# Kernel tuning notes

Measured on AMD Instinct MI355X. Metric: run time of the kernel, lower is better.

## Reference

```python
import jax, jax.numpy as jnp
import numpy as np

ASPECT_RATIOS = jnp.array([0.5, 1.0, 2.0], dtype=jnp.float32)
SCALES = jnp.array([1.0, 2.0, 4.0, 8.0, 16.0], dtype=jnp.float32)
BASE_SIZE = 16
STRIDE = 16
NEG_OVERLAP = 0.3
POS_OVERLAP = 0.7
PADDING = 0.0
RPN_BATCH = 256
RPN_FG_FRACTION = 0.5


def _mkanchors(ws, hs, x_ctr, y_ctr):
    return jnp.stack([x_ctr - 0.5 * (ws - 1), y_ctr - 0.5 * (hs - 1),
                      x_ctr + 0.5 * (ws - 1), y_ctr + 0.5 * (hs - 1)], axis=-1)


def _base_anchors():
    w = h = float(BASE_SIZE)
    x_ctr = y_ctr = 0.5 * (BASE_SIZE - 1)
    size = w * h
    size_ratios = size / ASPECT_RATIOS
    ws = jnp.round(jnp.sqrt(size_ratios))
    hs = jnp.round(ws * ASPECT_RATIOS)
    ratio_anchors = _mkanchors(ws, hs, x_ctr, y_ctr)          # (R,4)
    rw = ratio_anchors[:, 2] - ratio_anchors[:, 0] + 1
    rh = ratio_anchors[:, 3] - ratio_anchors[:, 1] + 1
    rx = ratio_anchors[:, 0] + 0.5 * (rw - 1)
    ry = ratio_anchors[:, 1] + 0.5 * (rh - 1)
    ws2 = rw[:, None] * SCALES[None, :]                        # (R,S)
    hs2 = rh[:, None] * SCALES[None, :]
    anchors = _mkanchors(ws2, hs2, rx[:, None], ry[:, None])   # (R,S,4)
    return anchors.reshape(-1, 4)                              # (A=R*S,4)


def _shifted_anchors(r, c):
    base = _base_anchors()                                     # (A,4)
    sx = jnp.arange(c, dtype=jnp.float32) * STRIDE
    sy = jnp.arange(r, dtype=jnp.float32) * STRIDE
    SX, SY = jnp.meshgrid(sx, sy)                              # (r,c)
    shifts = jnp.stack([SX.ravel(), SY.ravel(), SX.ravel(), SY.ravel()], axis=1)
    return (shifts[:, None, :] + base[None, :, :]).reshape(-1, 4)  # (K=r*c*A,4)


def _iou(a, b):
    area_a = (a[:, 2] - a[:, 0] + 1) * (a[:, 3] - a[:, 1] + 1)
    area_b = (b[:, 2] - b[:, 0] + 1) * (b[:, 3] - b[:, 1] + 1)
    iw = jnp.minimum(a[:, None, 2], b[None, :, 2]) - jnp.maximum(a[:, None, 0], b[None, :, 0]) + 1
    ih = jnp.minimum(a[:, None, 3], b[None, :, 3]) - jnp.maximum(a[:, None, 1], b[None, :, 1]) + 1
    inter = jnp.maximum(iw, 0) * jnp.maximum(ih, 0)
    return inter / (area_a[:, None] + area_b[None, :] - inter)


def _bbox_transform(ex, gt):
    ew = ex[:, 2] - ex[:, 0] + 1.0
    eh = ex[:, 3] - ex[:, 1] + 1.0
    ecx = ex[:, 0] + 0.5 * ew
    ecy = ex[:, 1] + 0.5 * eh
    gw = gt[:, 2] - gt[:, 0] + 1.0
    gh = gt[:, 3] - gt[:, 1] + 1.0
    gcx = gt[:, 0] + 0.5 * gw
    gcy = gt[:, 1] + 0.5 * gh
    return jnp.stack([(gcx - ecx) / ew, (gcy - ecy) / eh,
                      jnp.log(gw / ew), jnp.log(gh / eh)], axis=1)


def reference(target_bounding_boxes, metadata, scores):
    meta = metadata[0]
    gt = target_bounding_boxes[0]                               # (G,4)
    r, c = scores.shape[1], scores.shape[2]
    anchors = _shifted_anchors(r, c)                            # (K,4)
    K = anchors.shape[0]
    h, w = meta[0], meta[1]

    # anchors fully inside the image (padding=0); outside anchors masked
    inside = ((anchors[:, 0] >= -PADDING) & (anchors[:, 1] >= -PADDING) &
              (anchors[:, 2] < w + PADDING) & (anchors[:, 3] < h + PADDING))

    clipped = jnp.stack([jnp.clip(anchors[:, 0], 0.0, w - 1),
                         jnp.clip(anchors[:, 1], 0.0, h - 1),
                         jnp.clip(anchors[:, 2], 0.0, w - 1),
                         jnp.clip(anchors[:, 3], 0.0, h - 1)], axis=1)

    overlaps = _iou(clipped, gt)                                # (K,G)
    overlaps = jnp.where(inside[:, None], overlaps, -1.0)       # ignore outside anchors
    argmax_overlaps = jnp.argmax(overlaps, axis=1)              # best gt per anchor
    max_overlaps = jnp.max(overlaps, axis=1)
    gt_argmax = jnp.argmax(overlaps, axis=0)                    # best anchor per gt

    labels = jnp.full((K,), -1.0, dtype=jnp.float32)
    labels = jnp.where(inside & (max_overlaps < NEG_OVERLAP), 0.0, labels)
    labels = labels.at[gt_argmax].set(1.0)                      # dedup handled by .set
    labels = jnp.where(inside & (max_overlaps >= POS_OVERLAP), 1.0, labels)
    labels = jnp.where(inside, labels, -1.0)                    # unmap fill=-1

    # deterministic subsampling (original shuffles randomly): keep first-by-index
    num_fg = int(RPN_FG_FRACTION * RPN_BATCH)
    pos = labels == 1.0
    pos_rank = jnp.cumsum(pos.astype(jnp.int32))
    labels = jnp.where(pos & (pos_rank > num_fg), -1.0, labels)
    num_pos = jnp.minimum(pos.sum(), num_fg)
    num_bg = RPN_BATCH - num_pos
    neg = labels == 0.0
    neg_rank = jnp.cumsum(neg.astype(jnp.int32))
    labels = jnp.where(neg & (neg_rank > num_bg), -1.0, labels)

    matched_gt = gt[argmax_overlaps]                            # (K,4) gather
    bbox_targets = _bbox_transform(clipped, matched_gt)
    bbox_targets = jnp.where(inside[:, None], bbox_targets, 0.0)  # unmap fill=0

    return anchors[None], bbox_targets[None], labels[None]


def setup_inputs() -> dict:
    key = jax.random.key(0)
    k1, k2 = jax.random.split(key)
    H = W = 1600
    G = 100
    r = c = H // STRIDE                                          # 100
    A = 15                                                       # 3 ratios * 5 scales
    xy = jax.random.uniform(k1, (G, 2), minval=0.0, maxval=1400.0)
    wh = jax.random.uniform(k2, (G, 2), minval=16.0, maxval=200.0)
    gt = jnp.concatenate([xy, xy + wh], axis=1)[None]            # (1,G,4)
    metadata = jnp.array([[float(H), float(W), 1.0]], dtype=jnp.float32)
    scores = jnp.zeros((1, r, c, A), dtype=jnp.float32)          # only shape is used
    return {"target_bounding_boxes": gt, "metadata": metadata, "scores": scores}
```

## Files before the change

### kernel.cpp

```cpp
#include <hip/hip_runtime.h>
#include <math.h>


#define NUM_A 15
#define NUM_FG 128
#define RPN_BATCH 256
#define BLOCK 256
#define BLOCK2 1024
#define M2 2
#define APB2 (BLOCK2 * M2)
#define MAXG 256
#define MAXNG 768
#define CHUNK 8

__device__ __forceinline__ void base_anchor(int a, float& bx1, float& by1,
                                            float& bx2, float& by2) {
    const float RW[3] = {23.f, 16.f, 11.f};
    const float RH[3] = {12.f, 16.f, 22.f};
    int i = a / 5;
    int j = a - i * 5;
    float sc = (float)(1 << j);
    float w = RW[i] * sc;
    float h = RH[i] * sc;
    bx1 = 7.5f - 0.5f * (w - 1.f);
    by1 = 7.5f - 0.5f * (h - 1.f);
    bx2 = 7.5f + 0.5f * (w - 1.f);
    by2 = 7.5f + 0.5f * (h - 1.f);
}

__device__ __forceinline__ void anchor_coords(int k, int c, float& x1, float& y1,
                                              float& x2, float& y2) {
    int a = k % NUM_A;
    int p = k / NUM_A;
    int xi = p % c;
    int yi = p / c;
    float bx1, by1, bx2, by2;
    base_anchor(a, bx1, by1, bx2, by2);
    float sx = (float)xi * 16.f;
    float sy = (float)yi * 16.f;
    x1 = sx + bx1;  y1 = sy + by1;
    x2 = sx + bx2;  y2 = sy + by2;
}

__device__ __forceinline__ unsigned long long packvk(float v, int k) {
    unsigned u = __float_as_uint(v);
    u = (u & 0x80000000u) ? ~u : (u | 0x80000000u);
    return ((unsigned long long)u << 32) | (unsigned)(~k);
}

__global__ void __launch_bounds__(BLOCK) k_main(
        const float* __restrict__ gt, const float* __restrict__ meta,
        float* __restrict__ out_anch, float* __restrict__ out_bb,
        float* __restrict__ out_lab, int* __restrict__ posc, int* __restrict__ negc,
        unsigned long long* __restrict__ pbest, int K, int c, int G) {
    __shared__ float4 s_gt[MAXG];
    __shared__ unsigned long long s_best[MAXG];
    __shared__ int swp[4], swn[4];
    int tid = threadIdx.x;
    int b = blockIdx.x;
    const float4* gtv = (const float4*)gt;
    for (int g = tid; g < G; g += BLOCK) {
        s_gt[g] = gtv[g];
        s_best[g] = 0ULL;
    }
    __syncthreads();

    int k = b * BLOCK + tid;
    bool valid = (k < K);
    float h = meta[0], w = meta[1];
    float wm1 = __fsub_rn(w, 1.f), hm1 = __fsub_rn(h, 1.f);

    float x1, y1, x2, y2;
    anchor_coords(k, c, x1, y1, x2, y2);
    if (valid) ((float4*)out_anch)[k] = make_float4(x1, y1, x2, y2);
    bool inside = (x1 >= 0.f) && (y1 >= 0.f) && (x2 < w) && (y2 < h);

    float cx1 = fminf(fmaxf(x1, 0.f), wm1);
    float cy1 = fminf(fmaxf(y1, 0.f), hm1);
    float cx2 = fminf(fmaxf(x2, 0.f), wm1);
    float cy2 = fminf(fmaxf(y2, 0.f), hm1);
    float area_a = __fmul_rn(__fadd_rn(__fsub_rn(cx2, cx1), 1.f),
                             __fadd_rn(__fsub_rn(cy2, cy1), 1.f));

    float maxv = -2.f;
    int arg = 0;
    if (valid && inside) {
        for (int g = 0; g < G; ++g) {
            float4 gb = s_gt[g];
            float iw = __fadd_rn(__fsub_rn(fminf(cx2, gb.z), fmaxf(cx1, gb.x)), 1.f);
            float ih = __fadd_rn(__fsub_rn(fminf(cy2, gb.w), fmaxf(cy1, gb.y)), 1.f);
            float inter = __fmul_rn(fmaxf(iw, 0.f), fmaxf(ih, 0.f));
            float v = 0.f;
            if (inter > 0.f) {
                float gw = __fadd_rn(__fsub_rn(gb.z, gb.x), 1.f);
                float gh = __fadd_rn(__fsub_rn(gb.w, gb.y), 1.f);
                float areab = __fmul_rn(gw, gh);
                float denom = __fsub_rn(__fadd_rn(area_a, areab), inter);
                v = __fdiv_rn(inter, denom);
                unsigned long long pk = packvk(v, k);
                unsigned cur_hi = ((volatile unsigned*)&s_best[g])[1];
                if ((unsigned)(pk >> 32) >= cur_hi)
                    atomicMax(&s_best[g], pk);
            }
            if (v > maxv) { maxv = v; arg = g; }
        }
    }

    float labf = -1.f;
    if (valid) {
        float t0 = 0.f, t1 = 0.f, t2 = 0.f, t3 = 0.f;
        if (inside) {
            labf = (maxv >= 0.7f) ? 1.f : (maxv < 0.3f ? 0.f : -1.f);
            float4 gb = s_gt[arg];
            float ew  = __fadd_rn(__fsub_rn(cx2, cx1), 1.f);
            float eh  = __fadd_rn(__fsub_rn(cy2, cy1), 1.f);
            float ecx = __fadd_rn(cx1, __fmul_rn(0.5f, ew));
            float ecy = __fadd_rn(cy1, __fmul_rn(0.5f, eh));
            float gw  = __fadd_rn(__fsub_rn(gb.z, gb.x), 1.f);
            float gh  = __fadd_rn(__fsub_rn(gb.w, gb.y), 1.f);
            float gcx = __fadd_rn(gb.x, __fmul_rn(0.5f, gw));
            float gcy = __fadd_rn(gb.y, __fmul_rn(0.5f, gh));
            t0 = __fdiv_rn(__fsub_rn(gcx, ecx), ew);
            t1 = __fdiv_rn(__fsub_rn(gcy, ecy), eh);
            t2 = logf(__fdiv_rn(gw, ew));
            t3 = logf(__fdiv_rn(gh, eh));
        }
        ((float4*)out_bb)[k] = make_float4(t0, t1, t2, t3);
        out_lab[k] = labf;
    }

    bool pos = valid && (labf == 1.f);
    bool neg = valid && (labf == 0.f);
    unsigned long long bp = __ballot(pos ? 1 : 0);
    unsigned long long bn = __ballot(neg ? 1 : 0);
    int lane = tid & 63, wid = tid >> 6;
    if (lane == 0) { swp[wid] = __popcll(bp); swn[wid] = __popcll(bn); }
    __syncthreads();
    if (tid == 0) {
        posc[b] = swp[0] + swp[1] + swp[2] + swp[3];
        negc[b] = swn[0] + swn[1] + swn[2] + swn[3];
    }
    for (int g = tid; g < G; g += BLOCK)
        pbest[(size_t)b * G + g] = s_best[g];
}

__global__ void __launch_bounds__(BLOCK2) k_tail(
        float* __restrict__ out_lab, const int* __restrict__ posc,
        const int* __restrict__ negc, const unsigned long long* __restrict__ pbest,
        int K, int G, int NG) {
    __shared__ unsigned long long s_best[MAXG];
    __shared__ int s_kstar[MAXG];
    __shared__ int s_off_p[MAXNG], s_off_n[MAXNG];
    __shared__ int sp[BLOCK2], sn[BLOCK2];
    __shared__ unsigned char s_star[APB2];
    __shared__ int s_nbg;
    __shared__ int swp[16], swn[16];
    int tid = threadIdx.x;
    int b = blockIdx.x;
    int base = b * APB2;

    for (int i = tid; i < MAXNG; i += BLOCK2) { s_off_p[i] = 0; s_off_n[i] = 0; }
    for (int i = tid; i < APB2; i += BLOCK2) s_star[i] = 0;
    for (int g = tid; g < G; g += BLOCK2) s_best[g] = 0ULL;
    __syncthreads();

    int NT = NG * G;
    int R = BLOCK2 % G;
    int jr[CHUNK];
    jr[0] = 0;
    #pragma unroll
    for (int j = 1; j < CHUNK; ++j) {
        jr[j] = jr[j - 1] + R;
        if (jr[j] >= G) jr[j] -= G;
    }
    int g0 = tid % G;
    int stepg = (CHUNK * BLOCK2) % G;
    int e = tid;
    for (; e + (CHUNK - 1) * BLOCK2 < NT; e += CHUNK * BLOCK2) {
        unsigned long long u[CHUNK];
        #pragma unroll
        for (int j = 0; j < CHUNK; ++j) u[j] = pbest[e + j * BLOCK2];
        #pragma unroll
        for (int j = 0; j < CHUNK; ++j) {
            if (u[j] != 0ULL) {
                int g = g0 + jr[j];
                if (g >= G) g -= G;
                unsigned cur_hi = ((volatile unsigned*)&s_best[g])[1];
                if ((unsigned)(u[j] >> 32) >= cur_hi)
                    atomicMax(&s_best[g], u[j]);
            }
        }
        g0 += stepg;
        if (g0 >= G) g0 -= G;
    }
    for (; e < NT; e += BLOCK2) {
        unsigned long long u = pbest[e];
        if (u != 0ULL) {
            unsigned cur_hi = ((volatile unsigned*)&s_best[g0])[1];
            if ((unsigned)(u >> 32) >= cur_hi)
                atomicMax(&s_best[g0], u);
        }
        g0 += R;
        if (g0 >= G) g0 -= G;
    }
    __syncthreads();

    int ks = -1;
    if (tid < G) {
        unsigned long long v = s_best[tid];
        if (v != 0ULL) ks = (int)(~(unsigned)(v & 0xffffffffu));
    }
    if (tid < MAXG) s_kstar[tid] = (tid < G) ? ks : -1;
    __syncthreads();

    if (tid < G && ks >= 0 && ks >= base && ks < base + APB2)
        s_star[ks - base] = 1;

    if (tid < G && ks >= 0) {
        bool mine = true;
        for (int j = 0; j < tid; ++j)
            if (s_kstar[j] == ks) { mine = false; break; }
        if (mine) {
            float oldl = out_lab[ks];
            if (oldl != 1.f) {
                int grp = ks >> 8;
                atomicAdd(&s_off_p[grp], 1);
                if (oldl == 0.f) atomicAdd(&s_off_n[grp], -1);
            }
        }
    }
    __syncthreads();

    int myp = (tid < NG) ? posc[tid] + s_off_p[tid] : 0;
    int myn = (tid < NG) ? negc[tid] + s_off_n[tid] : 0;
    __syncthreads();
    sp[tid] = myp; sn[tid] = myn;
    __syncthreads();
    int vp = myp, vn = myn;
    for (int off = 1; off < BLOCK2; off <<= 1) {
        int ap = 0, an = 0;
        if (tid >= off) { ap = sp[tid - off]; an = sn[tid - off]; }
        __syncthreads();
        vp += ap; vn += an;
        sp[tid] = vp; sn[tid] = vn;
        __syncthreads();
    }
    if (tid < NG) { s_off_p[tid] = vp - myp; s_off_n[tid] = vn - myn; }
    if (tid == BLOCK2 - 1) {
        int total_pos = vp;
        int np = total_pos < NUM_FG ? total_pos : NUM_FG;
        s_nbg = RPN_BATCH - np;
    }
    __syncthreads();

    int lane = tid & 63, wid = tid >> 6;
    unsigned long long lm = (1ULL << lane) - 1ULL;
    int nbg = s_nbg;
    for (int i = 0; i < M2; ++i) {
        int k = base + i * BLOCK2 + tid;
        bool valid = (k < K);
        float lv = valid ? out_lab[k] : -1.f;
        if (valid && s_star[i * BLOCK2 + tid]) lv = 1.f;
        bool pos = valid && (lv == 1.f);
        bool neg = valid && (lv == 0.f);
        unsigned long long bp = __ballot(pos ? 1 : 0);
        unsigned long long bn = __ballot(neg ? 1 : 0);
        if (lane == 0) { swp[wid] = __popcll(bp); swn[wid] = __popcll(bn); }
        __syncthreads();
        int w0 = (tid >> 8) << 2;
        int poff = 0, noff = 0;
        for (int wv = w0; wv < wid; ++wv) { poff += swp[wv]; noff += swn[wv]; }
        int grp = (base + i * BLOCK2 + (tid >> 8) * 256) >> 8;
        int prank = s_off_p[grp] + poff + __popcll(bp & lm) + 1;
        int nrank = s_off_n[grp] + noff + __popcll(bn & lm) + 1;
        float fin = lv;
        if (pos && prank > NUM_FG) fin = -1.f;
        if (neg && nrank > nbg)    fin = -1.f;
        if (valid) out_lab[k] = fin;
        __syncthreads();
    }
}

extern "C" void kernel_launch(void* const* d_in, const int* in_sizes, int n_in,
                              void* d_out, int out_size, void* d_ws, size_t ws_size,
                              hipStream_t stream) {
    const float* gt   = (const float*)d_in[0];
    const float* meta = (const float*)d_in[1];
    int G  = in_sizes[0] / 4;
    int rc = in_sizes[2] / NUM_A;
    int c = 1;
    while ((long long)(c + 1) * (c + 1) <= (long long)rc) ++c;
    int K  = rc * NUM_A;
    int NG = (K + BLOCK - 1) / BLOCK;
    int NB2 = (K + APB2 - 1) / APB2;

    float* out      = (float*)d_out;
    float* out_anch = out;
    float* out_bb   = out + (size_t)4 * K;
    float* out_lab  = out + (size_t)8 * K;

    unsigned long long* pbest = (unsigned long long*)d_ws;
    int* posc  = (int*)(pbest + (size_t)MAXNG * MAXG);
    int* negc  = posc + MAXNG;

    hipLaunchKernelGGL(k_main, dim3(NG), dim3(BLOCK), 0, stream,
                       gt, meta, out_anch, out_bb, out_lab, posc, negc, pbest, K, c, G);
    hipLaunchKernelGGL(k_tail, dim3(NB2), dim3(BLOCK2), 0, stream,
                       out_lab, posc, negc, pbest, K, G, NG);
}
```

Baseline: 113.0 us.

## Use wave-shuffle scan in tail kernel and one anchor chunk per block

The tail kernel's block-wide prefix sum over per-group counts, which used shared memory and two barriers per step across ten steps, becomes a two-level wavefront shuffle scan with only a few barriers. Each block now handles 1024 anchors instead of 2048, so the grid doubles and the inner loop disappears. The cost is that every block redundantly repeats the per-block GT reduction and scan work, and there are now twice as many such blocks.

```diff
diff --git a/kernel.cpp b/kernel.cpp
--- a/kernel.cpp
+++ b/kernel.cpp
@@ -7,8 +7,7 @@
 #define RPN_BATCH 256
 #define BLOCK 256
 #define BLOCK2 1024
-#define M2 2
-#define APB2 (BLOCK2 * M2)
+#define APB2 BLOCK2
 #define MAXG 256
 #define MAXNG 768
 #define CHUNK 8
@@ -150,17 +149,18 @@
         int K, int G, int NG) {
     __shared__ unsigned long long s_best[MAXG];
     __shared__ int s_kstar[MAXG];
-    __shared__ int s_off_p[MAXNG], s_off_n[MAXNG];
-    __shared__ int sp[BLOCK2], sn[BLOCK2];
+    __shared__ int s_offp[MAXNG], s_offn[MAXNG];
     __shared__ unsigned char s_star[APB2];
+    __shared__ int s_wsp[16], s_wsn[16];
+    __shared__ int s_wop[16], s_won[16];
     __shared__ int s_nbg;
-    __shared__ int swp[16], swn[16];
     int tid = threadIdx.x;
     int b = blockIdx.x;
     int base = b * APB2;
-
-    for (int i = tid; i < MAXNG; i += BLOCK2) { s_off_p[i] = 0; s_off_n[i] = 0; }
-    for (int i = tid; i < APB2; i += BLOCK2) s_star[i] = 0;
+    int lane = tid & 63, wid = tid >> 6;
+
+    for (int i = tid; i < MAXNG; i += BLOCK2) { s_offp[i] = 0; s_offn[i] = 0; }
+    if (tid < APB2) s_star[tid] = 0;
     for (int g = tid; g < G; g += BLOCK2) s_best[g] = 0ULL;
     __syncthreads();
 
@@ -224,61 +224,72 @@
             float oldl = out_lab[ks];
             if (oldl != 1.f) {
                 int grp = ks >> 8;
-                atomicAdd(&s_off_p[grp], 1);
-                if (oldl == 0.f) atomicAdd(&s_off_n[grp], -1);
+                atomicAdd(&s_offp[grp], 1);
+                if (oldl == 0.f) atomicAdd(&s_offn[grp], -1);
             }
         }
     }
     __syncthreads();
 
-    int myp = (tid < NG) ? posc[tid] + s_off_p[tid] : 0;
-    int myn = (tid < NG) ? negc[tid] + s_off_n[tid] : 0;
-    __syncthreads();
-    sp[tid] = myp; sn[tid] = myn;
+    int myp = (tid < NG) ? posc[tid] + s_offp[tid] : 0;
+    int myn = (tid < NG) ? negc[tid] + s_offn[tid] : 0;
     __syncthreads();
     int vp = myp, vn = myn;
-    for (int off = 1; off < BLOCK2; off <<= 1) {
-        int ap = 0, an = 0;
-        if (tid >= off) { ap = sp[tid - off]; an = sn[tid - off]; }
-        __syncthreads();
-        vp += ap; vn += an;
-        sp[tid] = vp; sn[tid] = vn;
-        __syncthreads();
-    }
-    if (tid < NG) { s_off_p[tid] = vp - myp; s_off_n[tid] = vn - myn; }
-    if (tid == BLOCK2 - 1) {
-        int total_pos = vp;
-        int np = total_pos < NUM_FG ? total_pos : NUM_FG;
-        s_nbg = RPN_BATCH - np;
-    }
-    __syncthreads();
-
-    int lane = tid & 63, wid = tid >> 6;
+    #pragma unroll
+    for (int off = 1; off < 64; off <<= 1) {
+        int ap = __shfl_up(vp, off);
+        int an = __shfl_up(vn, off);
+        if (lane >= off) { vp += ap; vn += an; }
+    }
+    if (lane == 63) { s_wsp[wid] = vp; s_wsn[wid] = vn; }
+    __syncthreads();
+    if (tid < 16) {
+        int tp = s_wsp[tid], tn = s_wsn[tid];
+        int ip = tp, in_ = tn;
+        #pragma unroll
+        for (int off = 1; off < 16; off <<= 1) {
+            int ap = __shfl_up(ip, off);
+            int an = __shfl_up(in_, off);
+            if (lane >= off) { ip += ap; in_ += an; }
+        }
+        s_wop[tid] = ip - tp;
+        s_won[tid] = in_ - tn;
+        if (tid == 15) {
+            int total_pos = ip;
+            int np = total_pos < NUM_FG ? total_pos : NUM_FG;
+            s_nbg = RPN_BATCH - np;
+        }
+    }
+    __syncthreads();
+    if (tid < NG) {
+        s_offp[tid] = s_wop[wid] + vp - myp;
+        s_offn[tid] = s_won[wid] + vn - myn;
+    }
+    __syncthreads();
+
+    int k = base + tid;
+    bool valid = (k < K);
+    float lv = valid ? out_lab[k] : -1.f;
+    if (valid && s_star[tid]) lv = 1.f;
+    bool pos = valid && (lv == 1.f);
+    bool neg = valid && (lv == 0.f);
+    unsigned long long bp = __ballot(pos ? 1 : 0);
+    unsigned long long bn = __ballot(neg ? 1 : 0);
+    if (lane == 0) { s_wsp[wid] = __popcll(bp); s_wsn[wid] = __popcll(bn); }
+    __syncthreads();
+    int grp4 = tid >> 8;
+    int w0 = grp4 << 2;
+    int poff = 0, noff = 0;
+    for (int wv = w0; wv < wid; ++wv) { poff += s_wsp[wv]; noff += s_wsn[wv]; }
     unsigned long long lm = (1ULL << lane) - 1ULL;
+    int grp = (b << 2) + grp4;
+    int prank = s_offp[grp] + poff + __popcll(bp & lm) + 1;
+    int nrank = s_offn[grp] + noff + __popcll(bn & lm) + 1;
     int nbg = s_nbg;
-    for (int i = 0; i < M2; ++i) {
-        int k = base + i * BLOCK2 + tid;
-        bool valid = (k < K);
-        float lv = valid ? out_lab[k] : -1.f;
-        if (valid && s_star[i * BLOCK2 + tid]) lv = 1.f;
-        bool pos = valid && (lv == 1.f);
-        bool neg = valid && (lv == 0.f);
-        unsigned long long bp = __ballot(pos ? 1 : 0);
-        unsigned long long bn = __ballot(neg ? 1 : 0);
-        if (lane == 0) { swp[wid] = __popcll(bp); swn[wid] = __popcll(bn); }
-        __syncthreads();
-        int w0 = (tid >> 8) << 2;
-        int poff = 0, noff = 0;
-        for (int wv = w0; wv < wid; ++wv) { poff += swp[wv]; noff += swn[wv]; }
-        int grp = (base + i * BLOCK2 + (tid >> 8) * 256) >> 8;
-        int prank = s_off_p[grp] + poff + __popcll(bp & lm) + 1;
-        int nrank = s_off_n[grp] + noff + __popcll(bn & lm) + 1;
-        float fin = lv;
-        if (pos && prank > NUM_FG) fin = -1.f;
-        if (neg && nrank > nbg)    fin = -1.f;
-        if (valid) out_lab[k] = fin;
-        __syncthreads();
-    }
+    float fin = lv;
+    if (pos && prank > NUM_FG) fin = -1.f;
+    if (neg && nrank > nbg)    fin = -1.f;
+    if (valid) out_lab[k] = fin;
 }
 
 extern "C" void kernel_launch(void* const* d_in, const int* in_sizes, int n_in,
```

Result: no change. 112.0 us (-0.8%).
